# Performance work log

Hardware: AMD Instinct MI355X
Metric: run time of the kernel (lower is better)

Reference implementation:

```python
import jax, jax.numpy as jnp
import numpy as np

D_P, D_T, D_F = 128, 256, 384
D = D_P + D_T + D_F            # 768
NUM_PART, NUM_TIMES, NUM_F0 = 64, 601, 360
NHEAD, NLAYERS, DFF = 12, 6, 2048
CTX, PRED = 1024, 64
BATCH = 8
NEG = -1e9


def sin_emb(vals, d, L, base=10000.0):
    # vectorized version of the per-scalar sin_embedding loop
    i = jnp.arange(d // 2, dtype=jnp.float32)
    wk = base ** (-i / d) * (d / L)
    ang = vals[..., None].astype(jnp.float32) * wk           # [..., d/2]
    return jnp.stack([jnp.sin(ang), jnp.cos(ang)], axis=-1).reshape(vals.shape + (d,))


def layernorm(x, g, b, eps=1e-5):
    mu = jnp.mean(x, axis=-1, keepdims=True)
    var = jnp.var(x, axis=-1, keepdims=True)
    return (x - mu) * jax.lax.rsqrt(var + eps) * g + b


def setup_inputs() -> dict:
    key = jax.random.key(0)
    ks = jax.random.split(key, 20)
    inp = {}
    inp['context_participant'] = jax.random.randint(ks[0], (BATCH, CTX), 0, NUM_PART)
    inp['context_time'] = jax.random.uniform(ks[1], (BATCH, CTX), jnp.float32) * 60.0
    inp['context_f0'] = jax.random.randint(ks[2], (BATCH, CTX), 0, NUM_F0)
    # learned / frozen tables
    inp['part_table'] = jax.random.normal(ks[3], (NUM_PART, D_P), jnp.float32)
    inp['time_table'] = sin_emb(jnp.arange(NUM_TIMES, dtype=jnp.float32), D_T, NUM_TIMES)
    inp['f0_table'] = sin_emb(jnp.arange(NUM_F0, dtype=jnp.float32), D_F, NUM_F0)
    inp['pad'] = jax.random.normal(ks[4], (D,), jnp.float32)
    s = 0.02
    inp['Wqkv'] = jax.random.normal(ks[5], (NLAYERS, 3 * D, D), jnp.float32) * s
    inp['bqkv'] = jnp.zeros((NLAYERS, 3 * D), jnp.float32)
    inp['Wo'] = jax.random.normal(ks[6], (NLAYERS, D, D), jnp.float32) * s
    inp['bo'] = jnp.zeros((NLAYERS, D), jnp.float32)
    inp['ln1_g'] = jnp.ones((NLAYERS, D), jnp.float32)
    inp['ln1_b'] = jnp.zeros((NLAYERS, D), jnp.float32)
    inp['W1'] = jax.random.normal(ks[7], (NLAYERS, DFF, D), jnp.float32) * s
    inp['b1'] = jnp.zeros((NLAYERS, DFF), jnp.float32)
    inp['W2'] = jax.random.normal(ks[8], (NLAYERS, D, DFF), jnp.float32) * s
    inp['b2'] = jnp.zeros((NLAYERS, D), jnp.float32)
    inp['ln2_g'] = jnp.ones((NLAYERS, D), jnp.float32)
    inp['ln2_b'] = jnp.zeros((NLAYERS, D), jnp.float32)
    return inp


def reference(context_participant, context_time, context_f0, part_table, time_table,
              f0_table, pad, Wqkv, bqkv, Wo, bo, ln1_g, ln1_b, W1, b1, W2, b2,
              ln2_g, ln2_b):
    B = context_participant.shape[0]
    emb = jnp.concatenate([
        part_table[context_participant],
        sin_emb(context_time, D_T, NUM_TIMES),
        f0_table[context_f0],
    ], axis=-1)                                               # [B, CTX, D]
    dummy = jnp.broadcast_to(pad[None, None, :], (B, PRED, D))
    x = jnp.concatenate([emb, dummy], axis=1)                 # [B, S, D]
    S = CTX + PRED
    # causal mask with -1e9 above diagonal; target block fully masked (incl. diag)
    mask = jnp.where(jnp.triu(jnp.ones((S, S), bool), k=1), NEG, 0.0).astype(jnp.float32)
    mask = mask.at[CTX:, CTX:].set(NEG)
    hd = D // NHEAD
    scale = 1.0 / jnp.sqrt(jnp.float32(hd))
    for l in range(NLAYERS):
        qkv = x @ Wqkv[l].T + bqkv[l]
        q, k, v = jnp.split(qkv, 3, axis=-1)
        q = q.reshape(B, S, NHEAD, hd)
        k = k.reshape(B, S, NHEAD, hd)
        v = v.reshape(B, S, NHEAD, hd)
        scores = jnp.einsum('bqhd,bkhd->bhqk', q, k) * scale + mask
        attn = jax.nn.softmax(scores, axis=-1)
        ctx = jnp.einsum('bhqk,bkhd->bqhd', attn, v).reshape(B, S, D)
        x = layernorm(x + (ctx @ Wo[l].T + bo[l]), ln1_g[l], ln1_b[l])
        ff = jax.nn.relu(x @ W1[l].T + b1[l]) @ W2[l].T + b2[l]
        x = layernorm(x + ff, ln2_g[l], ln2_b[l])
    pred = x[:, CTX:, :]
    pred_cat_logits = pred[:, :, :D_P] @ part_table.T
    pred_time_logits = pred[:, :, D_P:D_P + D_T] @ time_table.T
    pred_f0_logits = pred[:, :, D_P + D_T:] @ f0_table.T
    return (pred_cat_logits, pred_time_logits, pred_f0_logits)
```

## Files before the change

kernel.cpp:

```cpp
#include <hip/hip_runtime.h>
#include <hip/hip_bf16.h>
#include <math.h>

#define D_P 128
#define D_T 256
#define D_F 384
#define DIM 768
#define NUM_TIMES 601
#define NUM_F0 360
#define NHEAD 12
#define HD 64
#define NLAYERS 6
#define DFF 2048
#define CTX 1024
#define SEQ 1088
#define BATCH 8
#define ROWS (BATCH*SEQ)
#define TDIM3 (3*DIM)
#define PREDROWS 512

typedef unsigned short ushort_t;
typedef __attribute__((ext_vector_type(8))) short bfrag;
typedef __attribute__((ext_vector_type(4))) float f32x4;

__global__ void SequenceModel_30425548325019_kernel(unsigned short* out, int n, unsigned short v) {
  int i = blockIdx.x * 256 + threadIdx.x;
  if (i < n) out[i] = v;
}

__device__ inline short f2bf(float f) {
  unsigned u = __float_as_uint(f);
  unsigned r = (u + 0x7FFFu + ((u >> 16) & 1u)) >> 16;
  return (short)r;
}

__device__ inline float bflo(unsigned u) { return __uint_as_float(u << 16); }
__device__ inline float bfhi(unsigned u) { return __uint_as_float(u & 0xFFFF0000u); }
__device__ inline unsigned packbf(float a, float b) {
  return ((unsigned)(ushort_t)f2bf(a)) | (((unsigned)(ushort_t)f2bf(b)) << 16);
}

__device__ inline void gload16(const void* g, void* l) {
  __builtin_amdgcn_global_load_lds(
      (const __attribute__((address_space(1))) unsigned*)g,
      (__attribute__((address_space(3))) unsigned*)l, 16, 0, 0);
}

__global__ __launch_bounds__(256) void cvt_bf16(const float* __restrict__ src,
                                                ushort_t* __restrict__ dst, int n) {
  int i = (blockIdx.x * 256 + threadIdx.x) * 4;
  if (i >= n) return;
  float4 v = *(const float4*)(src + i);
  dst[i + 0] = (ushort_t)f2bf(v.x);
  dst[i + 1] = (ushort_t)f2bf(v.y);
  dst[i + 2] = (ushort_t)f2bf(v.z);
  dst[i + 3] = (ushort_t)f2bf(v.w);
}

__global__ __launch_bounds__(256) void embed_kernel(
    const int* __restrict__ cp, const float* __restrict__ ct,
    const int* __restrict__ cf, const float* __restrict__ part,
    const float* __restrict__ f0t, const float* __restrict__ pad,
    ushort_t* __restrict__ xb) {
  int idx = blockIdx.x * 256 + threadIdx.x;
  if (idx >= ROWS * DIM) return;
  int d = idx % DIM;
  int row = idx / DIM;
  int b = row / SEQ, s = row - b * SEQ;
  float v;
  if (s >= CTX) {
    v = pad[d];
  } else if (d < D_P) {
    v = part[cp[b * CTX + s] * D_P + d];
  } else if (d < D_P + D_T) {
    int j = d - D_P;
    int i2 = j >> 1;
    float wk = powf(10000.f, -(float)i2 / (float)D_T) * ((float)D_T / (float)NUM_TIMES);
    float ang = ct[b * CTX + s] * wk;
    v = (j & 1) ? cosf(ang) : sinf(ang);
  } else {
    v = f0t[cf[b * CTX + s] * D_F + (d - D_P - D_T)];
  }
  xb[idx] = (ushort_t)f2bf(v);
}

#define BM 128
#define BN 128
#define BK 32
#define QSCALE 0.1803368801f

__global__ __launch_bounds__(256) void gemm_bb(
    const ushort_t* __restrict__ A, const ushort_t* __restrict__ B,
    const float* __restrict__ bias,
    float* __restrict__ C, ushort_t* __restrict__ Cb,
    int M, int N, int K, int relu, int qscale) {
  __shared__ short As[2][4 * BM * 8];
  __shared__ short Bs[2][4 * BN * 8];
  const int tid = threadIdx.x;
  const int wave = tid >> 6, lane = tid & 63;
  const int wr = wave >> 1, wc = wave & 1;
  const int l15 = lane & 15, l4 = lane >> 4;
  const int m0 = blockIdx.y * BM, n0 = blockIdx.x * BN;
  f32x4 acc[4][4] = {};

  const int u0row = (wave * 64 + lane) & 127, u0kg = (wave * 64 + lane) >> 7;
  const int u1row = (256 + wave * 64 + lane) & 127, u1kg = (256 + wave * 64 + lane) >> 7;
  const ushort_t* Ap0 = A + (size_t)(m0 + u0row) * K + u0kg * 8;
  const ushort_t* Bp0 = B + (size_t)(n0 + u0row) * K + u0kg * 8;
  const ushort_t* Ap1 = A + (size_t)(m0 + u1row) * K + u1kg * 8;
  const ushort_t* Bp1 = B + (size_t)(n0 + u1row) * K + u1kg * 8;
  const int ldsoff0 = (wave * 64) * 8;
  const int ldsoff1 = (256 + wave * 64) * 8;

  gload16(Ap0, &As[0][ldsoff0]);
  gload16(Bp0, &Bs[0][ldsoff0]);
  gload16(Ap1, &As[0][ldsoff1]);
  gload16(Bp1, &Bs[0][ldsoff1]);
  __syncthreads();

  int cur = 0;
  for (int k0 = 0; k0 < K; k0 += BK) {
    if (k0 + BK < K) {
      gload16(Ap0 + k0 + BK, &As[cur ^ 1][ldsoff0]);
      gload16(Bp0 + k0 + BK, &Bs[cur ^ 1][ldsoff0]);
      gload16(Ap1 + k0 + BK, &As[cur ^ 1][ldsoff1]);
      gload16(Bp1 + k0 + BK, &Bs[cur ^ 1][ldsoff1]);
    }
    bfrag a[4], b[4];
    #pragma unroll
    for (int f = 0; f < 4; ++f) {
      a[f] = *(const bfrag*)&As[cur][(l4 * BM + wr * 64 + f * 16 + l15) * 8];
      b[f] = *(const bfrag*)&Bs[cur][(l4 * BN + wc * 64 + f * 16 + l15) * 8];
    }
    __builtin_amdgcn_s_setprio(1);
    #pragma unroll
    for (int i = 0; i < 4; ++i)
      #pragma unroll
      for (int j = 0; j < 4; ++j)
        acc[i][j] = __builtin_amdgcn_mfma_f32_16x16x32_bf16(a[i], b[j], acc[i][j], 0, 0, 0);
    __builtin_amdgcn_s_setprio(0);
    __syncthreads();
    cur ^= 1;
  }
  #pragma unroll
  for (int i = 0; i < 4; ++i) {
    int mbase = m0 + wr * 64 + i * 16 + l4 * 4;
    #pragma unroll
    for (int j = 0; j < 4; ++j) {
      int n = n0 + wc * 64 + j * 16 + l15;
      float bv = bias[n];
      #pragma unroll
      for (int r = 0; r < 4; ++r) {
        int m = mbase + r;
        float v = acc[i][j][r] + bv;
        if (relu) v = fmaxf(v, 0.f);
        if (qscale && n < DIM) v *= QSCALE;
        if (C) C[(size_t)m * N + n] = v;
        if (Cb) Cb[(size_t)m * N + n] = (ushort_t)f2bf(v);
      }
    }
  }
}

__global__ __launch_bounds__(256) void gather_pred(const ushort_t* __restrict__ xb,
                                                   ushort_t* __restrict__ xpb) {
  int idx = blockIdx.x * 256 + threadIdx.x;
  if (idx >= PREDROWS * DIM) return;
  int r = idx / DIM, d = idx - r * DIM;
  int b = r >> 6, rr = r & 63;
  xpb[idx] = xb[(size_t)(b * SEQ + CTX + rr) * DIM + d];
}

__global__ __launch_bounds__(256) void head_mfma(
    const ushort_t* __restrict__ A, const ushort_t* __restrict__ B,
    float* __restrict__ C, int N, int K, int lda, int coloff) {
  __shared__ short As[4 * BM * 8];
  __shared__ short Bs[4 * BN * 8];
  const int tid = threadIdx.x;
  const int wave = tid >> 6, lane = tid & 63;
  const int wr = wave >> 1, wc = wave & 1;
  const int l15 = lane & 15, l4 = lane >> 4;
  const int m0 = blockIdx.y * BM, n0 = blockIdx.x * BN;
  f32x4 acc[4][4] = {};

  for (int k0 = 0; k0 < K; k0 += BK) {
    __syncthreads();
    #pragma unroll
    for (int i = 0; i < 2; ++i) {
      int u = i * 256 + wave * 64 + lane;
      int row = u & 127, kg = u >> 7;
      gload16(A + (size_t)(m0 + row) * lda + coloff + k0 + kg * 8,
              &As[(i * 256 + wave * 64) * 8]);
      gload16(B + (size_t)(n0 + row) * K + k0 + kg * 8,
              &Bs[(i * 256 + wave * 64) * 8]);
    }
    __syncthreads();
    bfrag a[4], b[4];
    #pragma unroll
    for (int f = 0; f < 4; ++f) {
      a[f] = *(const bfrag*)&As[(l4 * BM + wr * 64 + f * 16 + l15) * 8];
      b[f] = *(const bfrag*)&Bs[(l4 * BN + wc * 64 + f * 16 + l15) * 8];
    }
    #pragma unroll
    for (int i = 0; i < 4; ++i)
      #pragma unroll
      for (int j = 0; j < 4; ++j)
        acc[i][j] = __builtin_amdgcn_mfma_f32_16x16x32_bf16(a[i], b[j], acc[i][j], 0, 0, 0);
  }
  #pragma unroll
  for (int i = 0; i < 4; ++i) {
    int mbase = m0 + wr * 64 + i * 16 + l4 * 4;
    #pragma unroll
    for (int j = 0; j < 4; ++j) {
      int n = n0 + wc * 64 + j * 16 + l15;
      if (n >= N) continue;
      #pragma unroll
      for (int r = 0; r < 4; ++r)
        C[(size_t)(mbase + r) * N + n] = acc[i][j][r];
    }
  }
}

#define QBLK 64
#define KBLK 64
__global__ __launch_bounds__(256) void attn_mfma(const ushort_t* __restrict__ qkv,
                                                 ushort_t* __restrict__ outb) {
  const int qt = blockIdx.x, h = blockIdx.y, b = blockIdx.z;
  const int q0 = qt * QBLK;
  __shared__ char smem[8 * 64 * 9 * 2 * 2 > 64 * 65 * 4 ? 8 * 64 * 9 * 2 * 2 : 64 * 65 * 4];
  short* Vt = (short*)smem;
  short* Ps = (short*)(smem + 8 * 64 * 9 * 2);
  float* SO = (float*)smem;
  const int tid = threadIdx.x;
  const int wave = tid >> 6, lane = tid & 63;
  const int l15 = lane & 15, l4 = lane >> 4;
  const int qf = wave;

  const size_t qrow_addr = (size_t)(b * SEQ + q0 + qf * 16 + l15) * TDIM3 + h * HD;
  bfrag aq0 = *(const bfrag*)(qkv + qrow_addr + l4 * 8);
  bfrag aq1 = *(const bfrag*)(qkv + qrow_addr + 32 + l4 * 8);

  float mrun[4], lrun[4];
  #pragma unroll
  for (int r = 0; r < 4; ++r) { mrun[r] = -1e30f; lrun[r] = 0.f; }
  f32x4 o[4] = {};
  const int nkt = (q0 < CTX) ? (q0 + QBLK) / KBLK : (CTX / KBLK);

  for (int kt = 0; kt < nkt; ++kt) {
    const int k0 = kt * KBLK;
    __syncthreads();
    #pragma unroll
    for (int i = 0; i < 2; ++i) {
      int u = tid + 256 * i;
      int krow = u >> 3, dg = u & 7;
      bfrag vv = *(const bfrag*)(qkv + (size_t)(b * SEQ + k0 + krow) * TDIM3 + 2 * DIM + h * HD + dg * 8);
      int kg = krow >> 3, j = krow & 7;
      #pragma unroll
      for (int e = 0; e < 8; ++e)
        Vt[(kg * 64 + dg * 8 + e) * 9 + j] = vv[e];
    }
    f32x4 s[4];
    #pragma unroll
    for (int jk = 0; jk < 4; ++jk) {
      const size_t krow_addr = (size_t)(b * SEQ + k0 + jk * 16 + l15) * TDIM3 + DIM + h * HD;
      bfrag bk0 = *(const bfrag*)(qkv + krow_addr + l4 * 8);
      bfrag bk1 = *(const bfrag*)(qkv + krow_addr + 32 + l4 * 8);
      f32x4 acc = {};
      acc = __builtin_amdgcn_mfma_f32_16x16x32_bf16(aq0, bk0, acc, 0, 0, 0);
      s[jk] = __builtin_amdgcn_mfma_f32_16x16x32_bf16(aq1, bk1, acc, 0, 0, 0);
    }
    #pragma unroll
    for (int r = 0; r < 4; ++r) {
      const int qglob = q0 + qf * 16 + l4 * 4 + r;
      float pv[4];
      float tm = -1e30f;
      #pragma unroll
      for (int jk = 0; jk < 4; ++jk) {
        int kg = k0 + jk * 16 + l15;
        bool allowed = (qglob < CTX) ? (kg <= qglob) : true;
        pv[jk] = allowed ? s[jk][r] : -1e30f;
        tm = fmaxf(tm, pv[jk]);
      }
      tm = fmaxf(tm, __shfl_xor(tm, 1));
      tm = fmaxf(tm, __shfl_xor(tm, 2));
      tm = fmaxf(tm, __shfl_xor(tm, 4));
      tm = fmaxf(tm, __shfl_xor(tm, 8));
      float mn = fmaxf(mrun[r], tm);
      float alpha = exp2f(mrun[r] - mn);
      float ls = 0.f;
      #pragma unroll
      for (int jk = 0; jk < 4; ++jk) { pv[jk] = exp2f(pv[jk] - mn); ls += pv[jk]; }
      ls += __shfl_xor(ls, 1);
      ls += __shfl_xor(ls, 2);
      ls += __shfl_xor(ls, 4);
      ls += __shfl_xor(ls, 8);
      lrun[r] = lrun[r] * alpha + ls;
      mrun[r] = mn;
      #pragma unroll
      for (int df = 0; df < 4; ++df) o[df][r] *= alpha;
      const int qrow = qf * 16 + l4 * 4 + r;
      #pragma unroll
      for (int jk = 0; jk < 4; ++jk) {
        int kgi = jk * 2 + (l15 >> 3), j = l15 & 7;
        Ps[(kgi * 64 + qrow) * 9 + j] = f2bf(pv[jk]);
      }
    }
    __syncthreads();
    #pragma unroll
    for (int c = 0; c < 2; ++c) {
      bfrag pa = *(const bfrag*)&Ps[((c * 4 + l4) * 64 + qf * 16 + l15) * 9];
      #pragma unroll
      for (int df = 0; df < 4; ++df) {
        bfrag v = *(const bfrag*)&Vt[((c * 4 + l4) * 64 + df * 16 + l15) * 9];
        o[df] = __builtin_amdgcn_mfma_f32_16x16x32_bf16(pa, v, o[df], 0, 0, 0);
      }
    }
  }
  __syncthreads();
  #pragma unroll
  for (int r = 0; r < 4; ++r) {
    float li = 1.f / lrun[r];
    #pragma unroll
    for (int df = 0; df < 4; ++df)
      SO[(qf * 16 + l4 * 4 + r) * 65 + df * 16 + l15] = o[df][r] * li;
  }
  __syncthreads();
  #pragma unroll
  for (int i = 0; i < 2; ++i) {
    int s2 = tid + 256 * i;
    int r = s2 >> 3, kg = s2 & 7;
    ushort_t* dst = outb + (size_t)(b * SEQ + q0 + r) * DIM + h * HD + kg * 8;
    const float* sp = &SO[r * 65 + kg * 8];
    bfrag t;
    #pragma unroll
    for (int e = 0; e < 8; ++e) t[e] = f2bf(sp[e]);
    *(bfrag*)dst = t;
  }
}

__global__ __launch_bounds__(256) void ln_bb(const ushort_t* __restrict__ raw,
                                             ushort_t* __restrict__ xb,
                                             const float* __restrict__ g,
                                             const float* __restrict__ bb) {
  const int row = blockIdx.x;
  unsigned* pu = (unsigned*)(xb + (size_t)row * DIM);
  const unsigned* qu = (const unsigned*)(raw + (size_t)row * DIM);
  const float2* g2 = (const float2*)g;
  const float2* b2 = (const float2*)bb;
  const int tid = threadIdx.x;

  unsigned x0 = pu[tid], r0 = qu[tid];
  float v00 = bflo(x0) + bflo(r0);
  float v01 = bfhi(x0) + bfhi(r0);
  float v10 = 0.f, v11 = 0.f;
  if (tid < 128) {
    unsigned x1 = pu[256 + tid], r1 = qu[256 + tid];
    v10 = bflo(x1) + bflo(r1);
    v11 = bfhi(x1) + bfhi(r1);
  }
  float s1 = v00 + v01 + v10 + v11;
  float s2 = v00 * v00 + v01 * v01 + v10 * v10 + v11 * v11;
  #pragma unroll
  for (int off = 32; off >= 1; off >>= 1) {
    s1 += __shfl_down(s1, off);
    s2 += __shfl_down(s2, off);
  }
  __shared__ float r1s[4], r2s[4];
  int wid = tid >> 6;
  if ((tid & 63) == 0) { r1s[wid] = s1; r2s[wid] = s2; }
  __syncthreads();
  s1 = r1s[0] + r1s[1] + r1s[2] + r1s[3];
  s2 = r2s[0] + r2s[1] + r2s[2] + r2s[3];
  const float mu = s1 * (1.f / DIM);
  const float var = s2 * (1.f / DIM) - mu * mu;
  const float rs = rsqrtf(var + 1e-5f);
  float2 ga = g2[tid], ba = b2[tid];
  float o00 = (v00 - mu) * rs * ga.x + ba.x;
  float o01 = (v01 - mu) * rs * ga.y + ba.y;
  pu[tid] = packbf(o00, o01);
  if (tid < 128) {
    float2 gb = g2[256 + tid], bbv = b2[256 + tid];
    float o10 = (v10 - mu) * rs * gb.x + bbv.x;
    float o11 = (v11 - mu) * rs * gb.y + bbv.y;
    pu[256 + tid] = packbf(o10, o11);
  }
}

extern "C" void kernel_launch(void* const* d_in, const int* in_sizes, int n_in,
                              void* d_out, int out_size, void* d_ws, size_t ws_size,
                              hipStream_t stream) {
  const size_t N_XB   = (size_t)ROWS * DIM / 2;
  const size_t N_BUFB = (size_t)ROWS * TDIM3 / 2;
  const size_t N_CTB  = (size_t)ROWS * DIM / 2;
  const size_t N_WQ   = 10616832 / 2;
  const size_t N_WO   = 3538944 / 2;
  const size_t N_W1   = 9437184 / 2;
  const size_t N_W2   = 9437184 / 2;
  const size_t N_PT   = 8192 / 2;
  const size_t N_TT   = 153856 / 2;
  const size_t N_FT   = 138240 / 2;
  const size_t N_XPB  = (size_t)PREDROWS * DIM / 2;
  size_t need = (N_XB + N_BUFB + N_CTB + N_WQ + N_WO + N_W1 + N_W2 +
                 N_PT + N_TT + N_FT + N_XPB) * sizeof(float);
  if (ws_size < need) {
    SequenceModel_30425548325019_kernel<<<(out_size + 255) / 256, 256, 0, stream>>>(
        (unsigned short*)d_out, out_size, (unsigned short)0x4280);
    return;
  }

  const int*   cp    = (const int*)d_in[0];
  const float* ct    = (const float*)d_in[1];
  const int*   cf    = (const int*)d_in[2];
  const float* part  = (const float*)d_in[3];
  const float* timet = (const float*)d_in[4];
  const float* f0t   = (const float*)d_in[5];
  const float* pad   = (const float*)d_in[6];
  const float* Wqkv  = (const float*)d_in[7];
  const float* bqkv  = (const float*)d_in[8];
  const float* Wo    = (const float*)d_in[9];
  const float* bo    = (const float*)d_in[10];
  const float* ln1g  = (const float*)d_in[11];
  const float* ln1b  = (const float*)d_in[12];
  const float* W1    = (const float*)d_in[13];
  const float* b1    = (const float*)d_in[14];
  const float* W2    = (const float*)d_in[15];
  const float* b2    = (const float*)d_in[16];
  const float* ln2g  = (const float*)d_in[17];
  const float* ln2b  = (const float*)d_in[18];

  float* base = (float*)d_ws;
  ushort_t* xb     = (ushort_t*)base;      base += N_XB;
  ushort_t* bufb   = (ushort_t*)base;      base += N_BUFB;
  ushort_t* ctxbb  = (ushort_t*)base;      base += N_CTB;
  ushort_t* Wqkvb  = (ushort_t*)base;      base += N_WQ;
  ushort_t* Wob    = (ushort_t*)base;      base += N_WO;
  ushort_t* W1b    = (ushort_t*)base;      base += N_W1;
  ushort_t* W2b    = (ushort_t*)base;      base += N_W2;
  ushort_t* partb  = (ushort_t*)base;      base += N_PT;
  ushort_t* timetb = (ushort_t*)base;      base += N_TT;
  ushort_t* f0tb   = (ushort_t*)base;      base += N_FT;
  ushort_t* xpb    = (ushort_t*)base;

  cvt_bf16<<<(10616832 / 4 + 255) / 256, 256, 0, stream>>>(Wqkv, Wqkvb, 10616832);
  cvt_bf16<<<(3538944 / 4 + 255) / 256, 256, 0, stream>>>(Wo, Wob, 3538944);
  cvt_bf16<<<(9437184 / 4 + 255) / 256, 256, 0, stream>>>(W1, W1b, 9437184);
  cvt_bf16<<<(9437184 / 4 + 255) / 256, 256, 0, stream>>>(W2, W2b, 9437184);
  cvt_bf16<<<(8192 / 4 + 255) / 256, 256, 0, stream>>>(part, partb, 8192);
  cvt_bf16<<<(153856 / 4 + 255) / 256, 256, 0, stream>>>(timet, timetb, 153856);
  cvt_bf16<<<(138240 / 4 + 255) / 256, 256, 0, stream>>>(f0t, f0tb, 138240);

  embed_kernel<<<(ROWS * DIM + 255) / 256, 256, 0, stream>>>(cp, ct, cf, part, f0t, pad, xb);

  for (int l = 0; l < NLAYERS; ++l) {
    gemm_bb<<<dim3(TDIM3 / BN, ROWS / BM), 256, 0, stream>>>(
        xb, Wqkvb + (size_t)l * TDIM3 * DIM, bqkv + l * TDIM3,
        nullptr, bufb, ROWS, TDIM3, DIM, 0, 1);
    attn_mfma<<<dim3(SEQ / QBLK, NHEAD, BATCH), 256, 0, stream>>>(bufb, ctxbb);
    gemm_bb<<<dim3(DIM / BN, ROWS / BM), 256, 0, stream>>>(
        ctxbb, Wob + (size_t)l * DIM * DIM, bo + l * DIM,
        nullptr, bufb, ROWS, DIM, DIM, 0, 0);
    ln_bb<<<ROWS, 256, 0, stream>>>(bufb, xb, ln1g + l * DIM, ln1b + l * DIM);
    gemm_bb<<<dim3(DFF / BN, ROWS / BM), 256, 0, stream>>>(
        xb, W1b + (size_t)l * DFF * DIM, b1 + l * DFF,
        nullptr, bufb, ROWS, DFF, DIM, 1, 0);
    gemm_bb<<<dim3(DIM / BN, ROWS / BM), 256, 0, stream>>>(
        bufb, W2b + (size_t)l * DIM * DFF, b2 + l * DIM,
        nullptr, ctxbb, ROWS, DIM, DFF, 0, 0);
    ln_bb<<<ROWS, 256, 0, stream>>>(ctxbb, xb, ln2g + l * DIM, ln2b + l * DIM);
  }

  float* out = (float*)d_out;
  gather_pred<<<(PREDROWS * DIM + 255) / 256, 256, 0, stream>>>(xb, xpb);
  head_mfma<<<dim3(1, PREDROWS / BM), 256, 0, stream>>>(xpb, partb, out, 64, 128, DIM, 0);
  head_mfma<<<dim3(5, PREDROWS / BM), 256, 0, stream>>>(xpb, timetb, out + 32768, NUM_TIMES, 256, DIM, 128);
  head_mfma<<<dim3(3, PREDROWS / BM), 256, 0, stream>>>(xpb, f0tb, out + 32768 + 307712, NUM_F0, 384, DIM, 384);
}
```

Before: 2.744 ms.

## Store QKV in head-major planes so attention reads contiguous per-head rows

The QKV projection epilogue now scatters its output into a [3][batch][head][seq][64] layout instead of row-major [rows][2304]. The attention kernel then reads Q, K and V from contiguous per-head planes with a 128-byte row stride, so each K/V tile is a dense block and memory locality improves. The cost is an epilogue with integer divisions and scattered 2-byte stores in the GEMM. The unused fp32 output path is also removed.

```diff
diff --git a/kernel.cpp b/kernel.cpp
--- a/kernel.cpp
+++ b/kernel.cpp
@@ -92,8 +92,7 @@
 __global__ __launch_bounds__(256) void gemm_bb(
     const ushort_t* __restrict__ A, const ushort_t* __restrict__ B,
     const float* __restrict__ bias,
-    float* __restrict__ C, ushort_t* __restrict__ Cb,
-    int M, int N, int K, int relu, int qscale) {
+    ushort_t* __restrict__ Cb, int M, int N, int K, int relu, int mode) {
   __shared__ short As[2][4 * BM * 8];
   __shared__ short Bs[2][4 * BN * 8];
   const int tid = threadIdx.x;
@@ -149,14 +148,28 @@
     for (int j = 0; j < 4; ++j) {
       int n = n0 + wc * 64 + j * 16 + l15;
       float bv = bias[n];
-      #pragma unroll
-      for (int r = 0; r < 4; ++r) {
-        int m = mbase + r;
-        float v = acc[i][j][r] + bv;
-        if (relu) v = fmaxf(v, 0.f);
-        if (qscale && n < DIM) v *= QSCALE;
-        if (C) C[(size_t)m * N + n] = v;
-        if (Cb) Cb[(size_t)m * N + n] = (ushort_t)f2bf(v);
+      if (mode == 1) {
+        int idx = n / DIM;
+        int hh = (n - idx * DIM) >> 6;
+        int d = n & 63;
+        #pragma unroll
+        for (int r = 0; r < 4; ++r) {
+          int m = mbase + r;
+          int bb_ = m / SEQ, ss = m - bb_ * SEQ;
+          float v = acc[i][j][r] + bv;
+          if (idx == 0) v *= QSCALE;
+          size_t off = (((size_t)idx * BATCH + bb_) * NHEAD + hh) * ((size_t)SEQ * 64) +
+                       (size_t)ss * 64 + d;
+          Cb[off] = (ushort_t)f2bf(v);
+        }
+      } else {
+        #pragma unroll
+        for (int r = 0; r < 4; ++r) {
+          int m = mbase + r;
+          float v = acc[i][j][r] + bv;
+          if (relu) v = fmaxf(v, 0.f);
+          Cb[(size_t)m * N + n] = (ushort_t)f2bf(v);
+        }
       }
     }
   }
@@ -223,7 +236,7 @@
 
 #define QBLK 64
 #define KBLK 64
-__global__ __launch_bounds__(256) void attn_mfma(const ushort_t* __restrict__ qkv,
+__global__ __launch_bounds__(256) void attn_mfma(const ushort_t* __restrict__ qkvS,
                                                  ushort_t* __restrict__ outb) {
   const int qt = blockIdx.x, h = blockIdx.y, b = blockIdx.z;
   const int q0 = qt * QBLK;
@@ -236,9 +249,13 @@
   const int l15 = lane & 15, l4 = lane >> 4;
   const int qf = wave;
 
-  const size_t qrow_addr = (size_t)(b * SEQ + q0 + qf * 16 + l15) * TDIM3 + h * HD;
-  bfrag aq0 = *(const bfrag*)(qkv + qrow_addr + l4 * 8);
-  bfrag aq1 = *(const bfrag*)(qkv + qrow_addr + 32 + l4 * 8);
+  const size_t plane = (size_t)SEQ * 64;
+  const ushort_t* Qp = qkvS + ((size_t)(0 * BATCH + b) * NHEAD + h) * plane;
+  const ushort_t* Kp = qkvS + ((size_t)(1 * BATCH + b) * NHEAD + h) * plane;
+  const ushort_t* Vp = qkvS + ((size_t)(2 * BATCH + b) * NHEAD + h) * plane;
+
+  bfrag aq0 = *(const bfrag*)(Qp + (size_t)(q0 + qf * 16 + l15) * 64 + l4 * 8);
+  bfrag aq1 = *(const bfrag*)(Qp + (size_t)(q0 + qf * 16 + l15) * 64 + 32 + l4 * 8);
 
   float mrun[4], lrun[4];
   #pragma unroll
@@ -253,7 +270,7 @@
     for (int i = 0; i < 2; ++i) {
       int u = tid + 256 * i;
       int krow = u >> 3, dg = u & 7;
-      bfrag vv = *(const bfrag*)(qkv + (size_t)(b * SEQ + k0 + krow) * TDIM3 + 2 * DIM + h * HD + dg * 8);
+      bfrag vv = *(const bfrag*)(Vp + (size_t)(k0 + krow) * 64 + dg * 8);
       int kg = krow >> 3, j = krow & 7;
       #pragma unroll
       for (int e = 0; e < 8; ++e)
@@ -262,9 +279,9 @@
     f32x4 s[4];
     #pragma unroll
     for (int jk = 0; jk < 4; ++jk) {
-      const size_t krow_addr = (size_t)(b * SEQ + k0 + jk * 16 + l15) * TDIM3 + DIM + h * HD;
-      bfrag bk0 = *(const bfrag*)(qkv + krow_addr + l4 * 8);
-      bfrag bk1 = *(const bfrag*)(qkv + krow_addr + 32 + l4 * 8);
+      const ushort_t* kr = Kp + (size_t)(k0 + jk * 16 + l15) * 64;
+      bfrag bk0 = *(const bfrag*)(kr + l4 * 8);
+      bfrag bk1 = *(const bfrag*)(kr + 32 + l4 * 8);
       f32x4 acc = {};
       acc = __builtin_amdgcn_mfma_f32_16x16x32_bf16(aq0, bk0, acc, 0, 0, 0);
       s[jk] = __builtin_amdgcn_mfma_f32_16x16x32_bf16(aq1, bk1, acc, 0, 0, 0);
@@ -454,18 +471,18 @@
   for (int l = 0; l < NLAYERS; ++l) {
     gemm_bb<<<dim3(TDIM3 / BN, ROWS / BM), 256, 0, stream>>>(
         xb, Wqkvb + (size_t)l * TDIM3 * DIM, bqkv + l * TDIM3,
-        nullptr, bufb, ROWS, TDIM3, DIM, 0, 1);
+        bufb, ROWS, TDIM3, DIM, 0, 1);
     attn_mfma<<<dim3(SEQ / QBLK, NHEAD, BATCH), 256, 0, stream>>>(bufb, ctxbb);
     gemm_bb<<<dim3(DIM / BN, ROWS / BM), 256, 0, stream>>>(
         ctxbb, Wob + (size_t)l * DIM * DIM, bo + l * DIM,
-        nullptr, bufb, ROWS, DIM, DIM, 0, 0);
+        bufb, ROWS, DIM, DIM, 0, 0);
     ln_bb<<<ROWS, 256, 0, stream>>>(bufb, xb, ln1g + l * DIM, ln1b + l * DIM);
     gemm_bb<<<dim3(DFF / BN, ROWS / BM), 256, 0, stream>>>(
         xb, W1b + (size_t)l * DFF * DIM, b1 + l * DFF,
-        nullptr, bufb, ROWS, DFF, DIM, 1, 0);
+        bufb, ROWS, DFF, DIM, 1, 0);
     gemm_bb<<<dim3(DIM / BN, ROWS / BM), 256, 0, stream>>>(
         bufb, W2b + (size_t)l * DIM * DFF, b2 + l * DIM,
-        nullptr, ctxbb, ROWS, DIM, DFF, 0, 0);
+        ctxbb, ROWS, DIM, DFF, 0, 0);
     ln_bb<<<ROWS, 256, 0, stream>>>(ctxbb, xb, ln2g + l * DIM, ln2b + l * DIM);
   }
 
```

New measurement: 2.792 ms. About the same (+1.7%).
